# Kernel optimization log

Hardware: AMD Instinct MI355X
Metric: run time of the kernel (lower is better)

## Reference

```python
import jax, jax.numpy as jnp
import numpy as np

DIM = 512
PDIM = 64
NUM_HEAD = 8
HEAD_DIM = DIM // NUM_HEAD
SCALE = HEAD_DIM ** -0.5
EPS = 1e-6


def setup_inputs() -> dict:
    key = jax.random.key(0)
    ks = jax.random.split(key, 8)
    B, N = 8, 2048
    x_token = jax.random.normal(ks[0], (B, N, DIM), dtype=jnp.float32)
    x_path = jax.random.normal(ks[1], (B, N, PDIM), dtype=jnp.float32)
    idx_cluster = jax.random.randint(ks[2], (B, N), 0, 16, dtype=jnp.int32)
    # weights stored as [in, out] (y = x @ W + b), matching torch Linear math
    Wqk = jax.random.normal(ks[3], (DIM, 2 * DIM), dtype=jnp.float32) * 0.02
    Wv = jax.random.normal(ks[4], (DIM, DIM), dtype=jnp.float32) * 0.02
    Wpv = jax.random.normal(ks[5], (PDIM, PDIM), dtype=jnp.float32) * 0.02
    Wproj = jax.random.normal(ks[6], (DIM, DIM), dtype=jnp.float32) * 0.02
    bproj = jax.random.normal(ks[7], (DIM,), dtype=jnp.float32) * 0.02
    return {"x_token": x_token, "x_path": x_path, "idx_cluster": idx_cluster,
            "cluster_num": 16, "Wqk": Wqk, "Wv": Wv, "Wpv": Wpv,
            "Wproj": Wproj, "bproj": bproj}


def reference(x_token, x_path, idx_cluster, cluster_num, Wqk, Wv, Wpv, Wproj, bproj):
    B, N, C = x_token.shape
    qk = x_token @ Wqk                      # [B,N,2C]
    q, k = qk[..., :C], qk[..., C:]
    v = x_token @ Wv                        # [B,N,C]
    pv = x_path @ Wpv                       # dead code in original; kept for fidelity

    idx_shuffle = jnp.argsort(idx_cluster, axis=1)          # [B,N]
    idx_restore = jnp.argsort(idx_shuffle, axis=1)

    v_s = jnp.take_along_axis(v, idx_shuffle[..., None], axis=1)
    pv_s = jnp.take_along_axis(pv, idx_shuffle[..., None], axis=1)  # unused (faithful)

    attn_map = jnp.einsum('bic,bjc->bij', q, k) * SCALE     # [B,N,N]

    # torch does two gathers, both with dim=1; the second index is constant along
    # rows, so attn2[b,i,j] = attn_map[b, idx_shuffle[b, idx_shuffle[b,j]], j]
    double = jnp.take_along_axis(idx_shuffle, idx_shuffle, axis=1)  # [B,N]
    col_vals = jnp.take_along_axis(jnp.swapaxes(attn_map, 1, 2), double[..., None], axis=2)[..., 0]  # [B,N]
    attn = jnp.broadcast_to(col_vals[:, None, :], (B, N, N))

    # contiguous per-cluster block mask in sorted order == equality of sorted ids
    s = jnp.sort(idx_cluster, axis=1)
    mask = (s[:, :, None] == s[:, None, :]) & (s[:, :, None] < cluster_num)

    attn = jnp.where(mask, attn, jnp.float32(-1e9))
    attn = jnp.exp(attn.astype(jnp.float32))
    attn = (attn + EPS / N) / (jnp.sum(attn, axis=-1, keepdims=True) + EPS)

    out = attn @ v_s                                         # [B,N,C]
    out = jnp.swapaxes(out, 1, 2).reshape(B, N, C)           # faithful layout scramble
    out = jnp.take_along_axis(out, idx_restore[..., None], axis=1)
    x_out = out @ Wproj + bproj
    return x_out, attn_map
```

## Files before the change

### kernel.cpp

```cpp
#include <hip/hip_runtime.h>
#include <hip/hip_bf16.h>

typedef __attribute__((ext_vector_type(8))) short short8;
typedef __attribute__((ext_vector_type(4))) float floatx4;

__device__ __forceinline__ unsigned short f2bfu(float f) {
    unsigned u = __float_as_uint(f);
    unsigned rounding = 0x7fffu + ((u >> 16) & 1u);
    return (unsigned short)((u + rounding) >> 16);
}
__device__ __forceinline__ float bfu2f(unsigned short u) {
    return __uint_as_float(((unsigned)u) << 16);
}

__device__ __forceinline__ void async_ld16(const void* g, void* l) {
    __builtin_amdgcn_global_load_lds(
        (const __attribute__((address_space(1))) void*)g,
        (__attribute__((address_space(3))) void*)l, 16, 0, 0);
}

#define B_  8
#define N_  2048
#define C_  512
#define NC_ 16

__global__ __launch_bounds__(256) void cvt_x(const float4* __restrict__ x,
                                             unsigned short* __restrict__ xbf) {
    size_t i = (size_t)blockIdx.x * 256 + threadIdx.x;
    float4 f = x[i];
    unsigned short u0 = f2bfu(f.x), u1 = f2bfu(f.y), u2 = f2bfu(f.z), u3 = f2bfu(f.w);
    uint2 p;
    p.x = (unsigned)u0 | ((unsigned)u1 << 16);
    p.y = (unsigned)u2 | ((unsigned)u3 << 16);
    *(uint2*)(xbf + 4 * i) = p;
}

__global__ __launch_bounds__(256) void cvt_wqkv(const float* __restrict__ Wqk,
                                                const float* __restrict__ Wv,
                                                unsigned short* __restrict__ WT) {
    int id = blockIdx.x * 256 + threadIdx.x;
    int n = id >> 9, k = id & 511;
    float v = (n < 1024) ? Wqk[(size_t)k * 1024 + n] : Wv[(size_t)k * 512 + (n - 1024)];
    WT[id] = f2bfu(v);
}

__global__ __launch_bounds__(256) void cvt_wproj(const float* __restrict__ W,
                                                 unsigned short* __restrict__ WT) {
    int id = blockIdx.x * 256 + threadIdx.x;
    int n = id >> 9, k = id & 511;
    WT[id] = f2bfu(W[(size_t)k * 512 + n]);
}

__global__ __launch_bounds__(256) void sort_kernel(const int* __restrict__ idx_cluster,
                                                   int* __restrict__ shuf,
                                                   int* __restrict__ restore,
                                                   int* __restrict__ svals,
                                                   int* __restrict__ dbl,
                                                   int* __restrict__ cstart) {
    int b = blockIdx.x, t = threadIdx.x;
    __shared__ int vals[N_];
    __shared__ int seghist[256 * 17];
    __shared__ int cbase[NC_], ctot[NC_];
    __shared__ int shufs[N_];
    const int* src = idx_cluster + (size_t)b * N_;
    for (int j = t; j < N_; j += 256) vals[j] = src[j];
    for (int c = 0; c < NC_; ++c) seghist[t * 17 + c] = 0;
    __syncthreads();
    for (int i = 0; i < 8; ++i) {
        int c = vals[t * 8 + i];
        seghist[t * 17 + c]++;
    }
    __syncthreads();
    if (t < NC_) {
        int run = 0;
        for (int s = 0; s < 256; ++s) {
            int x = seghist[s * 17 + t];
            seghist[s * 17 + t] = run;
            run += x;
        }
        ctot[t] = run;
    }
    __syncthreads();
    if (t == 0) {
        int run = 0;
        for (int c = 0; c < NC_; ++c) {
            cbase[c] = run;
            cstart[b * 17 + c] = run;
            run += ctot[c];
        }
        cstart[b * 17 + NC_] = run;
    }
    __syncthreads();
    for (int i = 0; i < 8; ++i) {
        int p = t * 8 + i;
        int c = vals[p];
        int pos = cbase[c] + seghist[t * 17 + c];
        seghist[t * 17 + c]++;
        shufs[pos] = p;
    }
    __syncthreads();
    for (int j = t; j < N_; j += 256) {
        int sj = shufs[j];
        shuf[(size_t)b * N_ + j] = sj;
        svals[(size_t)b * N_ + j] = vals[sj];
        restore[(size_t)b * N_ + sj] = j;
        dbl[(size_t)b * N_ + j] = shufs[sj];
    }
}

template <int MODE>
__global__ __launch_bounds__(256) void gemm_bt(const unsigned short* __restrict__ A,
                                               const unsigned short* __restrict__ Bt,
                                               float* __restrict__ outF,
                                               unsigned short* __restrict__ outQ,
                                               unsigned short* __restrict__ outK,
                                               unsigned short* __restrict__ outV,
                                               const float* __restrict__ bias) {
    constexpr int K = 512;
    int t = threadIdx.x;
    int lane = t & 63, wave = t >> 6;
    int wm = (wave & 1) * 64, wn = (wave >> 1) * 64;
    int m0 = blockIdx.y * 128, n0 = blockIdx.x * 128;
    if (MODE == 1) {
        size_t b = blockIdx.z;
        A += b * (size_t)N_ * 512;
        Bt += b * (size_t)N_ * 512;
        outF += b * (size_t)N_ * N_;
    }
    __shared__ __align__(16) unsigned short As[128 * 64];
    __shared__ __align__(16) unsigned short Bs[128 * 64];
    floatx4 acc[4][4] = {};
    int l15 = lane & 15, q4 = lane >> 4;
    int srow = lane >> 3, schk = lane & 7;
    int sgc = schk ^ srow;
    int xr = l15 & 7;

    for (int k0 = 0; k0 < K; k0 += 64) {
        __syncthreads();
#pragma unroll
        for (int i = 0; i < 4; ++i) {
            int cid = i * 4 + wave;
            int row = cid * 8 + srow;
            async_ld16(A + (size_t)(m0 + row) * 512 + k0 + sgc * 8, (char*)As + cid * 1024);
            async_ld16(Bt + (size_t)(n0 + row) * 512 + k0 + sgc * 8, (char*)Bs + cid * 1024);
        }
        __syncthreads();
#pragma unroll
        for (int kk = 0; kk < 2; ++kk) {
            int csw = (((kk * 4 + q4) ^ xr) * 8);
            short8 af[4], bfr[4];
#pragma unroll
            for (int mi = 0; mi < 4; ++mi)
                af[mi] = *(const short8*)(&As[(wm + mi * 16 + l15) * 64 + csw]);
#pragma unroll
            for (int ni = 0; ni < 4; ++ni)
                bfr[ni] = *(const short8*)(&Bs[(wn + ni * 16 + l15) * 64 + csw]);
#pragma unroll
            for (int mi = 0; mi < 4; ++mi)
#pragma unroll
                for (int ni = 0; ni < 4; ++ni)
                    acc[mi][ni] = __builtin_amdgcn_mfma_f32_16x16x32_bf16(af[mi], bfr[ni], acc[mi][ni], 0, 0, 0);
        }
    }
#pragma unroll
    for (int mi = 0; mi < 4; ++mi) {
#pragma unroll
        for (int ni = 0; ni < 4; ++ni) {
#pragma unroll
            for (int r = 0; r < 4; ++r) {
                int row = m0 + wm + mi * 16 + q4 * 4 + r;
                int col = n0 + wn + ni * 16 + l15;
                float v = acc[mi][ni][r];
                if (MODE == 0) {
                    unsigned short u = f2bfu(v);
                    if (col < 512)       outQ[(size_t)row * 512 + col] = u;
                    else if (col < 1024) outK[(size_t)row * 512 + col - 512] = u;
                    else                 outV[(size_t)row * 512 + col - 1024] = u;
                } else if (MODE == 1) {
                    outF[(size_t)row * N_ + col] = v * 0.125f;
                } else {
                    outF[(size_t)row * 512 + col] = v + bias[col];
                }
            }
        }
    }
}

__global__ __launch_bounds__(256) void cluster_reduce(const float* __restrict__ attn,
                                                      const int* __restrict__ shuf,
                                                      const int* __restrict__ dbl,
                                                      const int* __restrict__ cstart,
                                                      const unsigned short* __restrict__ vbf,
                                                      float* __restrict__ Ot) {
    int c = blockIdx.x, b = blockIdx.y, t = threadIdx.x;
    int start = cstart[b * 17 + c], end = cstart[b * 17 + c + 1];
    int n = end - start;
    if (n <= 0) return;
    __shared__ float e_lds[N_];
    __shared__ float Sred;
    if (t == 0) Sred = 0.f;
    __syncthreads();
    float ps = 0.f;
    for (int i = t; i < n; i += 256) {
        int j = start + i;
        int dj = dbl[(size_t)b * N_ + j];
        float cv = attn[(size_t)b * N_ * N_ + (size_t)dj * N_ + j];
        float e = expf(cv);
        e_lds[i] = e;
        ps += e;
    }
    atomicAdd(&Sred, ps);
    __syncthreads();
    float t0 = 0.f, t1 = 0.f;
    for (int i = 0; i < n; ++i) {
        float e = e_lds[i];
        int row = shuf[(size_t)b * N_ + start + i];
        const unsigned short* vr = vbf + ((size_t)b * N_ + row) * 512;
        t0 += e * bfu2f(vr[t]);
        t1 += e * bfu2f(vr[t + 256]);
    }
    float inv = 1.f / Sred;
    Ot[((size_t)b * 512 + t) * 16 + c] = t0 * inv;
    Ot[((size_t)b * 512 + t + 256) * 16 + c] = t1 * inv;
}

__global__ __launch_bounds__(256) void build_out3(const float* __restrict__ Ot,
                                                  const int* __restrict__ svals,
                                                  const int* __restrict__ restore,
                                                  unsigned int* __restrict__ out3u) {
    int rg = blockIdx.x, b = blockIdx.y, t = threadIdx.x;
    __shared__ float Olds[512 * 16];
    __shared__ int slds[N_];
    for (int i = t; i < 512 * 16; i += 256) Olds[i] = Ot[(size_t)b * 512 * 16 + i];
    for (int i = t; i < N_; i += 256) slds[i] = svals[(size_t)b * N_ + i];
    __syncthreads();
    for (int n = rg * 64; n < rg * 64 + 64; ++n) {
        int r = restore[(size_t)b * N_ + n];
        int rq = r >> 2;
        int bj = (r & 3) * 512;
        int c0 = slds[bj + 2 * t];
        int c1 = slds[bj + 2 * t + 1];
        float v0 = Olds[rq * 16 + c0];
        float v1 = Olds[rq * 16 + c1];
        unsigned p = (unsigned)f2bfu(v0) | ((unsigned)f2bfu(v1) << 16);
        out3u[((size_t)b * N_ + n) * 256 + t] = p;
    }
}

extern "C" void kernel_launch(void* const* d_in, const int* in_sizes, int n_in,
                              void* d_out, int out_size, void* d_ws, size_t ws_size,
                              hipStream_t stream) {
    const float* x_token = (const float*)d_in[0];
    const int* idx_cluster = (const int*)d_in[2];
    const float* Wqk = (const float*)d_in[4];
    const float* Wv = (const float*)d_in[5];
    const float* Wproj = (const float*)d_in[7];
    const float* bproj = (const float*)d_in[8];

    float* x_out = (float*)d_out;
    float* attn = x_out + (size_t)B_ * N_ * C_;

    char* ws = (char*)d_ws;
    size_t off = 0;
    auto alloc = [&](size_t bytes) {
        void* p = ws + off;
        off += (bytes + 255) & ~(size_t)255;
        return p;
    };
    unsigned short* WqkvT = (unsigned short*)alloc(1536 * 512 * 2);
    unsigned short* WprojT = (unsigned short*)alloc(512 * 512 * 2);
    unsigned short* xbf = (unsigned short*)alloc((size_t)B_ * N_ * C_ * 2);
    unsigned short* qbf = (unsigned short*)alloc((size_t)B_ * N_ * C_ * 2);
    unsigned short* kbf = (unsigned short*)alloc((size_t)B_ * N_ * C_ * 2);
    unsigned short* vbf = (unsigned short*)alloc((size_t)B_ * N_ * C_ * 2);
    int* shuf = (int*)alloc((size_t)B_ * N_ * 4);
    int* restore = (int*)alloc((size_t)B_ * N_ * 4);
    int* svals = (int*)alloc((size_t)B_ * N_ * 4);
    int* dbl = (int*)alloc((size_t)B_ * N_ * 4);
    int* cstart = (int*)alloc(B_ * 17 * 4);
    float* Ot = (float*)alloc((size_t)B_ * 512 * 16 * 4);

    cvt_x<<<dim3((B_ * N_ * C_) / (256 * 4)), dim3(256), 0, stream>>>((const float4*)x_token, xbf);
    cvt_wqkv<<<dim3((1536 * 512) / 256), dim3(256), 0, stream>>>(Wqk, Wv, WqkvT);
    cvt_wproj<<<dim3((512 * 512) / 256), dim3(256), 0, stream>>>(Wproj, WprojT);

    sort_kernel<<<dim3(B_), dim3(256), 0, stream>>>(idx_cluster, shuf, restore, svals, dbl, cstart);

    gemm_bt<0><<<dim3(1536 / 128, 16384 / 128, 1), dim3(256), 0, stream>>>(
        xbf, WqkvT, nullptr, qbf, kbf, vbf, nullptr);

    gemm_bt<1><<<dim3(N_ / 128, N_ / 128, B_), dim3(256), 0, stream>>>(
        qbf, kbf, attn, nullptr, nullptr, nullptr, nullptr);

    cluster_reduce<<<dim3(NC_, B_), dim3(256), 0, stream>>>(attn, shuf, dbl, cstart, vbf, Ot);

    build_out3<<<dim3(N_ / 64, B_), dim3(256), 0, stream>>>(Ot, svals, restore, (unsigned int*)xbf);

    gemm_bt<2><<<dim3(512 / 128, 16384 / 128, 1), dim3(256), 0, stream>>>(
        xbf, WprojT, x_out, nullptr, nullptr, nullptr, bproj);
}
```

Before: 343.7 us.

## Replace output projection GEMM with cluster-grouped weight sums and split cluster reduction

Each output row is a gather from only 16 per-cluster values, so the projection is rewritten algebraically. Wproj rows are pre-summed per (batch, column-group, cluster) into a small grouped weight, and each output is computed as a 16-term dot product instead of running a full 512-wide GEMM. The per-cluster attention-value reduction is also split across 8 slices with a combine kernel, giving more parallel blocks. This adds extra kernels and partial buffers, and bf16 rounding of the summed weights changes numerics slightly.

```diff
diff --git a/kernel.cpp b/kernel.cpp
--- a/kernel.cpp
+++ b/kernel.cpp
@@ -23,6 +23,7 @@
 #define N_  2048
 #define C_  512
 #define NC_ 16
+#define SL_ 8
 
 __global__ __launch_bounds__(256) void cvt_x(const float4* __restrict__ x,
                                              unsigned short* __restrict__ xbf) {
@@ -42,13 +43,6 @@
     int n = id >> 9, k = id & 511;
     float v = (n < 1024) ? Wqk[(size_t)k * 1024 + n] : Wv[(size_t)k * 512 + (n - 1024)];
     WT[id] = f2bfu(v);
-}
-
-__global__ __launch_bounds__(256) void cvt_wproj(const float* __restrict__ W,
-                                                 unsigned short* __restrict__ WT) {
-    int id = blockIdx.x * 256 + threadIdx.x;
-    int n = id >> 9, k = id & 511;
-    WT[id] = f2bfu(W[(size_t)k * 512 + n]);
 }
 
 __global__ __launch_bounds__(256) void sort_kernel(const int* __restrict__ idx_cluster,
@@ -176,74 +170,129 @@
                     if (col < 512)       outQ[(size_t)row * 512 + col] = u;
                     else if (col < 1024) outK[(size_t)row * 512 + col - 512] = u;
                     else                 outV[(size_t)row * 512 + col - 1024] = u;
-                } else if (MODE == 1) {
+                } else {
                     outF[(size_t)row * N_ + col] = v * 0.125f;
-                } else {
-                    outF[(size_t)row * 512 + col] = v + bias[col];
                 }
             }
         }
     }
 }
 
-__global__ __launch_bounds__(256) void cluster_reduce(const float* __restrict__ attn,
-                                                      const int* __restrict__ shuf,
-                                                      const int* __restrict__ dbl,
-                                                      const int* __restrict__ cstart,
-                                                      const unsigned short* __restrict__ vbf,
-                                                      float* __restrict__ Ot) {
-    int c = blockIdx.x, b = blockIdx.y, t = threadIdx.x;
+__global__ __launch_bounds__(256) void cluster_reduce2(const float* __restrict__ attn,
+                                                       const int* __restrict__ shuf,
+                                                       const int* __restrict__ dbl,
+                                                       const int* __restrict__ cstart,
+                                                       const unsigned short* __restrict__ vbf,
+                                                       float* __restrict__ Opart,
+                                                       float* __restrict__ Spart) {
+    int c = blockIdx.x, b = blockIdx.y, sl = blockIdx.z, t = threadIdx.x;
     int start = cstart[b * 17 + c], end = cstart[b * 17 + c + 1];
     int n = end - start;
-    if (n <= 0) return;
-    __shared__ float e_lds[N_];
-    __shared__ float Sred;
-    if (t == 0) Sred = 0.f;
-    __syncthreads();
-    float ps = 0.f;
-    for (int i = t; i < n; i += 256) {
-        int j = start + i;
+    int i0 = (n * sl) / SL_, i1 = (n * (sl + 1)) / SL_;
+    int cnt = i1 - i0;
+    __shared__ float e_lds[256];
+    __shared__ int row_lds[256];
+    if (t < cnt) {
+        int j = start + i0 + t;
         int dj = dbl[(size_t)b * N_ + j];
-        float cv = attn[(size_t)b * N_ * N_ + (size_t)dj * N_ + j];
-        float e = expf(cv);
-        e_lds[i] = e;
-        ps += e;
-    }
-    atomicAdd(&Sred, ps);
-    __syncthreads();
-    float t0 = 0.f, t1 = 0.f;
-    for (int i = 0; i < n; ++i) {
+        float e = expf(attn[(size_t)b * N_ * N_ + (size_t)dj * N_ + j]);
+        e_lds[t] = e;
+        row_lds[t] = shuf[(size_t)b * N_ + j];
+    }
+    __syncthreads();
+    if (t == 0) {
+        float s = 0.f;
+        for (int i = 0; i < cnt; ++i) s += e_lds[i];
+        Spart[(b * SL_ + sl) * NC_ + c] = s;
+    }
+    float a0 = 0.f, a1 = 0.f;
+    for (int i = 0; i < cnt; ++i) {
         float e = e_lds[i];
-        int row = shuf[(size_t)b * N_ + start + i];
-        const unsigned short* vr = vbf + ((size_t)b * N_ + row) * 512;
-        t0 += e * bfu2f(vr[t]);
-        t1 += e * bfu2f(vr[t + 256]);
-    }
-    float inv = 1.f / Sred;
-    Ot[((size_t)b * 512 + t) * 16 + c] = t0 * inv;
-    Ot[((size_t)b * 512 + t + 256) * 16 + c] = t1 * inv;
-}
-
-__global__ __launch_bounds__(256) void build_out3(const float* __restrict__ Ot,
-                                                  const int* __restrict__ svals,
-                                                  const int* __restrict__ restore,
-                                                  unsigned int* __restrict__ out3u) {
-    int rg = blockIdx.x, b = blockIdx.y, t = threadIdx.x;
-    __shared__ float Olds[512 * 16];
-    __shared__ int slds[N_];
-    for (int i = t; i < 512 * 16; i += 256) Olds[i] = Ot[(size_t)b * 512 * 16 + i];
-    for (int i = t; i < N_; i += 256) slds[i] = svals[(size_t)b * N_ + i];
-    __syncthreads();
-    for (int n = rg * 64; n < rg * 64 + 64; ++n) {
-        int r = restore[(size_t)b * N_ + n];
-        int rq = r >> 2;
-        int bj = (r & 3) * 512;
-        int c0 = slds[bj + 2 * t];
-        int c1 = slds[bj + 2 * t + 1];
-        float v0 = Olds[rq * 16 + c0];
-        float v1 = Olds[rq * 16 + c1];
-        unsigned p = (unsigned)f2bfu(v0) | ((unsigned)f2bfu(v1) << 16);
-        out3u[((size_t)b * N_ + n) * 256 + t] = p;
+        unsigned u = *(const unsigned*)(vbf + ((size_t)b * N_ + row_lds[i]) * 512 + 2 * t);
+        a0 += e * bfu2f((unsigned short)u);
+        a1 += e * bfu2f((unsigned short)(u >> 16));
+    }
+    float2 o; o.x = a0; o.y = a1;
+    *(float2*)(Opart + (((size_t)(b * SL_ + sl) * NC_ + c) * 512 + 2 * t)) = o;
+}
+
+__global__ __launch_bounds__(256) void combine_O(const float* __restrict__ Opart,
+                                                 const float* __restrict__ Spart,
+                                                 float* __restrict__ Ot) {
+    int c = blockIdx.x, b = blockIdx.y, t = threadIdx.x;
+    float S = 0.f;
+    for (int sl = 0; sl < SL_; ++sl) S += Spart[(b * SL_ + sl) * NC_ + c];
+    float inv = S > 0.f ? 1.f / S : 0.f;
+    float a0 = 0.f, a1 = 0.f;
+    for (int sl = 0; sl < SL_; ++sl) {
+        float2 o = *(const float2*)(Opart + (((size_t)(b * SL_ + sl) * NC_ + c) * 512 + 2 * t));
+        a0 += o.x; a1 += o.y;
+    }
+    Ot[((size_t)b * 512 + 2 * t) * NC_ + c] = a0 * inv;
+    Ot[((size_t)b * 512 + 2 * t + 1) * NC_ + c] = a1 * inv;
+}
+
+__global__ __launch_bounds__(256) void build_wg(const float* __restrict__ Wproj,
+                                                const int* __restrict__ svals,
+                                                unsigned int* __restrict__ Wg) {
+    int g = blockIdx.x, b = blockIdx.y, t = threadIdx.x;
+    __shared__ int slds[512];
+    for (int i = t; i < 512; i += 256) slds[i] = svals[(size_t)b * N_ + g * 512 + i];
+    __syncthreads();
+    unsigned int* base = Wg + (size_t)(b * 4 + g) * NC_ * 256;
+#pragma unroll
+    for (int c = 0; c < NC_; ++c) base[c * 256 + t] = 0;
+    int ccur = slds[0];
+    float a0 = 0.f, a1 = 0.f;
+    for (int cd = 0; cd < 512; ++cd) {
+        int c = slds[cd];
+        if (c != ccur) {
+            base[ccur * 256 + t] = (unsigned)f2bfu(a0) | ((unsigned)f2bfu(a1) << 16);
+            a0 = 0.f; a1 = 0.f; ccur = c;
+        }
+        float2 w = *(const float2*)(Wproj + (size_t)cd * 512 + 2 * t);
+        a0 += w.x; a1 += w.y;
+    }
+    base[ccur * 256 + t] = (unsigned)f2bfu(a0) | ((unsigned)f2bfu(a1) << 16);
+}
+
+__global__ __launch_bounds__(256) void xout_kernel(const float* __restrict__ Ot,
+                                                   const unsigned int* __restrict__ Wg,
+                                                   const int* __restrict__ restore,
+                                                   const float* __restrict__ bias,
+                                                   float* __restrict__ xout) {
+    int nb = blockIdx.x, b = blockIdx.y, t = threadIdx.x;
+    int n0 = nb * 64;
+    __shared__ int r_lds[64];
+    if (t < 64) r_lds[t] = restore[(size_t)b * N_ + n0 + t];
+    __syncthreads();
+    float b0 = bias[2 * t], b1 = bias[2 * t + 1];
+    const float* Otb = Ot + (size_t)b * 512 * NC_;
+    for (int g = 0; g < 4; ++g) {
+        const unsigned int* wg = Wg + (size_t)(b * 4 + g) * NC_ * 256 + t;
+        float wx[NC_], wy[NC_];
+#pragma unroll
+        for (int c = 0; c < NC_; ++c) {
+            unsigned u = wg[c * 256];
+            wx[c] = bfu2f((unsigned short)u);
+            wy[c] = bfu2f((unsigned short)(u >> 16));
+        }
+        for (int i = 0; i < 64; ++i) {
+            int r = r_lds[i];
+            if ((r & 3) != g) continue;
+            int rq = r >> 2;
+            const float4* op = (const float4*)(Otb + rq * NC_);
+            float o[NC_];
+            *(float4*)&o[0]  = op[0];
+            *(float4*)&o[4]  = op[1];
+            *(float4*)&o[8]  = op[2];
+            *(float4*)&o[12] = op[3];
+            float a0 = b0, a1 = b1;
+#pragma unroll
+            for (int c = 0; c < NC_; ++c) { a0 += o[c] * wx[c]; a1 += o[c] * wy[c]; }
+            float2 res; res.x = a0; res.y = a1;
+            *(float2*)(xout + ((size_t)b * N_ + n0 + i) * 512 + 2 * t) = res;
+        }
     }
 }
 
@@ -268,7 +317,6 @@
         return p;
     };
     unsigned short* WqkvT = (unsigned short*)alloc(1536 * 512 * 2);
-    unsigned short* WprojT = (unsigned short*)alloc(512 * 512 * 2);
     unsigned short* xbf = (unsigned short*)alloc((size_t)B_ * N_ * C_ * 2);
     unsigned short* qbf = (unsigned short*)alloc((size_t)B_ * N_ * C_ * 2);
     unsigned short* kbf = (unsigned short*)alloc((size_t)B_ * N_ * C_ * 2);
@@ -278,13 +326,17 @@
     int* svals = (int*)alloc((size_t)B_ * N_ * 4);
     int* dbl = (int*)alloc((size_t)B_ * N_ * 4);
     int* cstart = (int*)alloc(B_ * 17 * 4);
-    float* Ot = (float*)alloc((size_t)B_ * 512 * 16 * 4);
+    float* Ot = (float*)alloc((size_t)B_ * 512 * NC_ * 4);
+    float* Opart = (float*)alloc((size_t)B_ * SL_ * NC_ * 512 * 4);
+    float* Spart = (float*)alloc((size_t)B_ * SL_ * NC_ * 4);
+    unsigned int* Wg = (unsigned int*)alloc((size_t)B_ * 4 * NC_ * 256 * 4);
 
     cvt_x<<<dim3((B_ * N_ * C_) / (256 * 4)), dim3(256), 0, stream>>>((const float4*)x_token, xbf);
     cvt_wqkv<<<dim3((1536 * 512) / 256), dim3(256), 0, stream>>>(Wqk, Wv, WqkvT);
-    cvt_wproj<<<dim3((512 * 512) / 256), dim3(256), 0, stream>>>(Wproj, WprojT);
 
     sort_kernel<<<dim3(B_), dim3(256), 0, stream>>>(idx_cluster, shuf, restore, svals, dbl, cstart);
+
+    build_wg<<<dim3(4, B_), dim3(256), 0, stream>>>(Wproj, svals, Wg);
 
     gemm_bt<0><<<dim3(1536 / 128, 16384 / 128, 1), dim3(256), 0, stream>>>(
         xbf, WqkvT, nullptr, qbf, kbf, vbf, nullptr);
@@ -292,10 +344,10 @@
     gemm_bt<1><<<dim3(N_ / 128, N_ / 128, B_), dim3(256), 0, stream>>>(
         qbf, kbf, attn, nullptr, nullptr, nullptr, nullptr);
 
-    cluster_reduce<<<dim3(NC_, B_), dim3(256), 0, stream>>>(attn, shuf, dbl, cstart, vbf, Ot);
-
-    build_out3<<<dim3(N_ / 64, B_), dim3(256), 0, stream>>>(Ot, svals, restore, (unsigned int*)xbf);
-
-    gemm_bt<2><<<dim3(512 / 128, 16384 / 128, 1), dim3(256), 0, stream>>>(
-        xbf, WprojT, x_out, nullptr, nullptr, nullptr, bproj);
-}
+    cluster_reduce2<<<dim3(NC_, B_, SL_), dim3(256), 0, stream>>>(
+        attn, shuf, dbl, cstart, vbf, Opart, Spart);
+
+    combine_O<<<dim3(NC_, B_), dim3(256), 0, stream>>>(Opart, Spart, Ot);
+
+    xout_kernel<<<dim3(N_ / 64, B_), dim3(256), 0, stream>>>(Ot, Wg, restore, bproj, x_out);
+}
```

Result: slower. 545.7 us (+58.8%).

## Apply Wv after cluster reduction instead of projecting V for every token

Applied to the files above, without the earlier changes.

Uses linearity to reduce the bf16 token features per cluster first, then multiplies the small per-cluster vectors by Wv in a new fp32 kernel. This drops the V third of the QKV projection GEMM and the V buffer writes and reads. It adds an extra small launch, and the order of reduction and projection changes the rounding of V.

```diff
diff --git a/kernel.cpp b/kernel.cpp
--- a/kernel.cpp
+++ b/kernel.cpp
@@ -35,13 +35,11 @@
     *(uint2*)(xbf + 4 * i) = p;
 }
 
-__global__ __launch_bounds__(256) void cvt_wqkv(const float* __restrict__ Wqk,
-                                                const float* __restrict__ Wv,
-                                                unsigned short* __restrict__ WT) {
+__global__ __launch_bounds__(256) void cvt_wqk(const float* __restrict__ Wqk,
+                                               unsigned short* __restrict__ WT) {
     int id = blockIdx.x * 256 + threadIdx.x;
     int n = id >> 9, k = id & 511;
-    float v = (n < 1024) ? Wqk[(size_t)k * 1024 + n] : Wv[(size_t)k * 512 + (n - 1024)];
-    WT[id] = f2bfu(v);
+    WT[id] = f2bfu(Wqk[(size_t)k * 1024 + n]);
 }
 
 __global__ __launch_bounds__(256) void cvt_wproj(const float* __restrict__ W,
@@ -114,7 +112,6 @@
                                                float* __restrict__ outF,
                                                unsigned short* __restrict__ outQ,
                                                unsigned short* __restrict__ outK,
-                                               unsigned short* __restrict__ outV,
                                                const float* __restrict__ bias) {
     constexpr int K = 512;
     int t = threadIdx.x;
@@ -173,9 +170,8 @@
                 float v = acc[mi][ni][r];
                 if (MODE == 0) {
                     unsigned short u = f2bfu(v);
-                    if (col < 512)       outQ[(size_t)row * 512 + col] = u;
-                    else if (col < 1024) outK[(size_t)row * 512 + col - 512] = u;
-                    else                 outV[(size_t)row * 512 + col - 1024] = u;
+                    if (col < 512) outQ[(size_t)row * 512 + col] = u;
+                    else           outK[(size_t)row * 512 + col - 512] = u;
                 } else if (MODE == 1) {
                     outF[(size_t)row * N_ + col] = v * 0.125f;
                 } else {
@@ -190,8 +186,8 @@
                                                       const int* __restrict__ shuf,
                                                       const int* __restrict__ dbl,
                                                       const int* __restrict__ cstart,
-                                                      const unsigned short* __restrict__ vbf,
-                                                      float* __restrict__ Ot) {
+                                                      const unsigned short* __restrict__ xbf,
+                                                      float* __restrict__ xe) {
     int c = blockIdx.x, b = blockIdx.y, t = threadIdx.x;
     int start = cstart[b * 17 + c], end = cstart[b * 17 + c + 1];
     int n = end - start;
@@ -215,13 +211,30 @@
     for (int i = 0; i < n; ++i) {
         float e = e_lds[i];
         int row = shuf[(size_t)b * N_ + start + i];
-        const unsigned short* vr = vbf + ((size_t)b * N_ + row) * 512;
-        t0 += e * bfu2f(vr[t]);
-        t1 += e * bfu2f(vr[t + 256]);
+        unsigned u = *(const unsigned*)(xbf + ((size_t)b * N_ + row) * 512 + 2 * t);
+        t0 += e * bfu2f((unsigned short)u);
+        t1 += e * bfu2f((unsigned short)(u >> 16));
     }
     float inv = 1.f / Sred;
-    Ot[((size_t)b * 512 + t) * 16 + c] = t0 * inv;
-    Ot[((size_t)b * 512 + t + 256) * 16 + c] = t1 * inv;
+    float2 r; r.x = t0 * inv; r.y = t1 * inv;
+    *(float2*)(xe + ((size_t)b * NC_ + c) * 512 + 2 * t) = r;
+}
+
+__global__ __launch_bounds__(256) void ovw_kernel(const float* __restrict__ xe,
+                                                  const float* __restrict__ Wv,
+                                                  float* __restrict__ Ot) {
+    int c = blockIdx.x, b = blockIdx.y, t = threadIdx.x;
+    __shared__ float xl[512];
+    for (int i = t; i < 512; i += 256) xl[i] = xe[((size_t)b * NC_ + c) * 512 + i];
+    __syncthreads();
+    float a0 = 0.f, a1 = 0.f;
+    for (int k = 0; k < 512; ++k) {
+        float xv = xl[k];
+        float2 w = *(const float2*)(Wv + (size_t)k * 512 + 2 * t);
+        a0 += xv * w.x; a1 += xv * w.y;
+    }
+    Ot[((size_t)b * 512 + 2 * t) * 16 + c] = a0;
+    Ot[((size_t)b * 512 + 2 * t + 1) * 16 + c] = a1;
 }
 
 __global__ __launch_bounds__(256) void build_out3(const float* __restrict__ Ot,
@@ -267,35 +280,37 @@
         off += (bytes + 255) & ~(size_t)255;
         return p;
     };
-    unsigned short* WqkvT = (unsigned short*)alloc(1536 * 512 * 2);
+    unsigned short* WqkT = (unsigned short*)alloc(1024 * 512 * 2);
     unsigned short* WprojT = (unsigned short*)alloc(512 * 512 * 2);
     unsigned short* xbf = (unsigned short*)alloc((size_t)B_ * N_ * C_ * 2);
     unsigned short* qbf = (unsigned short*)alloc((size_t)B_ * N_ * C_ * 2);
     unsigned short* kbf = (unsigned short*)alloc((size_t)B_ * N_ * C_ * 2);
-    unsigned short* vbf = (unsigned short*)alloc((size_t)B_ * N_ * C_ * 2);
     int* shuf = (int*)alloc((size_t)B_ * N_ * 4);
     int* restore = (int*)alloc((size_t)B_ * N_ * 4);
     int* svals = (int*)alloc((size_t)B_ * N_ * 4);
     int* dbl = (int*)alloc((size_t)B_ * N_ * 4);
     int* cstart = (int*)alloc(B_ * 17 * 4);
+    float* xe = (float*)alloc((size_t)B_ * NC_ * 512 * 4);
     float* Ot = (float*)alloc((size_t)B_ * 512 * 16 * 4);
 
     cvt_x<<<dim3((B_ * N_ * C_) / (256 * 4)), dim3(256), 0, stream>>>((const float4*)x_token, xbf);
-    cvt_wqkv<<<dim3((1536 * 512) / 256), dim3(256), 0, stream>>>(Wqk, Wv, WqkvT);
+    cvt_wqk<<<dim3((1024 * 512) / 256), dim3(256), 0, stream>>>(Wqk, WqkT);
     cvt_wproj<<<dim3((512 * 512) / 256), dim3(256), 0, stream>>>(Wproj, WprojT);
 
     sort_kernel<<<dim3(B_), dim3(256), 0, stream>>>(idx_cluster, shuf, restore, svals, dbl, cstart);
 
-    gemm_bt<0><<<dim3(1536 / 128, 16384 / 128, 1), dim3(256), 0, stream>>>(
-        xbf, WqkvT, nullptr, qbf, kbf, vbf, nullptr);
+    gemm_bt<0><<<dim3(1024 / 128, 16384 / 128, 1), dim3(256), 0, stream>>>(
+        xbf, WqkT, nullptr, qbf, kbf, nullptr);
 
     gemm_bt<1><<<dim3(N_ / 128, N_ / 128, B_), dim3(256), 0, stream>>>(
-        qbf, kbf, attn, nullptr, nullptr, nullptr, nullptr);
-
-    cluster_reduce<<<dim3(NC_, B_), dim3(256), 0, stream>>>(attn, shuf, dbl, cstart, vbf, Ot);
+        qbf, kbf, attn, nullptr, nullptr, nullptr);
+
+    cluster_reduce<<<dim3(NC_, B_), dim3(256), 0, stream>>>(attn, shuf, dbl, cstart, xbf, xe);
+
+    ovw_kernel<<<dim3(NC_, B_), dim3(256), 0, stream>>>(xe, Wv, Ot);
 
     build_out3<<<dim3(N_ / 64, B_), dim3(256), 0, stream>>>(Ot, svals, restore, (unsigned int*)xbf);
 
     gemm_bt<2><<<dim3(512 / 128, 16384 / 128, 1), dim3(256), 0, stream>>>(
-        xbf, WprojT, x_out, nullptr, nullptr, nullptr, bproj);
-}
+        xbf, WprojT, x_out, nullptr, nullptr, bproj);
+}
```

Result: slower. 355.8 us (+3.5%).
